# Optimization experiments

Hardware: AMD Instinct MI355X
Metric: run time of the kernel (lower is better)

## Reference

```python
import jax, jax.numpy as jnp
import numpy as np

WZ, WH, WW = 2, 6, 12  # window_size (Z, H, W)
NUM_HEADS = 6


def _layernorm(x, g, b, eps=1e-5):
    m = jnp.mean(x, axis=-1, keepdims=True)
    v = jnp.mean((x - m) ** 2, axis=-1, keepdims=True)
    return (x - m) * jax.lax.rsqrt(v + eps) * g + b


def setup_inputs() -> dict:
    key = jax.random.key(0)
    ks = jax.random.split(key, 8)
    B, Z, H, W, C = 1, 8, 91, 180, 192
    s = 0.02
    return {
        "x": jax.random.normal(ks[0], (B, Z * H * W, C), jnp.float32),
        "norm1_g": jnp.ones((C,), jnp.float32),
        "norm1_b": jnp.zeros((C,), jnp.float32),
        "qkv_w": jax.random.normal(ks[1], (3 * C, C), jnp.float32) * s,
        "qkv_b": jnp.zeros((3 * C,), jnp.float32),
        "proj_w": jax.random.normal(ks[2], (C, C), jnp.float32) * s,
        "proj_b": jnp.zeros((C,), jnp.float32),
        "norm2_g": jnp.ones((C,), jnp.float32),
        "norm2_b": jnp.zeros((C,), jnp.float32),
        "fc1_w": jax.random.normal(ks[3], (4 * C, C), jnp.float32) * s,
        "fc1_b": jnp.zeros((4 * C,), jnp.float32),
        "fc2_w": jax.random.normal(ks[4], (C, 4 * C), jnp.float32) * s,
        "fc2_b": jnp.zeros((C,), jnp.float32),
        "Z": Z, "H": H, "W": W, "roll": 1,
    }


def _forward(x, norm1_g, norm1_b, qkv_w, qkv_b, proj_w, proj_b,
             norm2_g, norm2_b, fc1_w, fc1_b, fc2_w, fc2_b, Z, H, W, roll):
    B, N, C = x.shape
    shortcut = x
    x = x.reshape(B, Z, H, W, C)
    # pad to window multiples (right-pad, as in torch F.pad)
    pz, ph, pw = (-Z) % WZ, (-H) % WH, (-W) % WW
    x = jnp.pad(x, ((0, 0), (0, pz), (0, ph), (0, pw), (0, 0)))
    Zp, Hp, Wp = Z + pz, H + ph, W + pw
    if roll:
        x = jnp.roll(x, (-(WZ // 2), -(WH // 2), -(WW // 2)), axis=(1, 2, 3))
    # window partition -> (B*nW, wz*wh*ww, C)
    x = x.reshape(B, Zp // WZ, WZ, Hp // WH, WH, Wp // WW, WW, C)
    x = x.transpose(0, 1, 3, 5, 2, 4, 6, 7).reshape(-1, WZ * WH * WW, C)
    xw = _layernorm(x, norm1_g, norm1_b)
    # windowed multi-head attention (mask is always None in this module)
    nw, L, _ = xw.shape
    hd = C // NUM_HEADS
    qkv = (xw @ qkv_w.T + qkv_b).reshape(nw, L, 3, NUM_HEADS, hd)
    q, k, v = jnp.moveaxis(qkv, 2, 0)        # each (nw, L, nh, hd)
    q = q * (hd ** -0.5)
    attn = jnp.einsum('nqhd,nkhd->nhqk', q, k)
    attn = jax.nn.softmax(attn, axis=-1)
    out = jnp.einsum('nhqk,nkhd->nqhd', attn, v).reshape(nw, L, C)
    out = out @ proj_w.T + proj_b
    # window reverse
    x = out.reshape(B, Zp // WZ, Hp // WH, Wp // WW, WZ, WH, WW, C)
    x = x.transpose(0, 1, 4, 2, 5, 3, 6, 7).reshape(B, Zp, Hp, Wp, C)
    if roll:
        x = jnp.roll(x, (WZ // 2, WH // 2, WW // 2), axis=(1, 2, 3))
    x = x[:, :Z, :H, :W, :].reshape(B, Z * H * W, C)
    x = shortcut + x
    # MLP with post-norm (as written in the source: x + norm2(mlp(x)))
    h = jax.nn.gelu(x @ fc1_w.T + fc1_b, approximate=False)
    h = h @ fc2_w.T + fc2_b
    return x + _layernorm(h, norm2_g, norm2_b)


def reference(x, norm1_g, norm1_b, qkv_w, qkv_b, proj_w, proj_b,
              norm2_g, norm2_b, fc1_w, fc1_b, fc2_w, fc2_b, Z, H, W, roll):
    return _forward(x, norm1_g, norm1_b, qkv_w, qkv_b, proj_w, proj_b,
                    norm2_g, norm2_b, fc1_w, fc1_b, fc2_w, fc2_b, Z, H, W, roll)
```

## Files before the change

kernel.cpp:

```cpp
#include <hip/hip_runtime.h>
#include <hip/hip_bf16.h>
#include <math.h>

#define C_DIM 192
#define NH 6
#define HD 32
#define L_WIN 144
#define NWIN 960
#define MROWS (NWIN * L_WIN)
#define NTOK 131040
#define Z_ 8
#define H_ 91
#define W_ 180
#define HP_ 96
#define WS_REQUIRED 212336640ull

#define OFF_WBF   0ull
#define OFF_XWC   1048576ull
#define OFF_QKVB  51367936ull
#define OFF_ATTNO 1048576ull
#define OFF_X1B   51367936ull
#define WO_QKV  0
#define WO_PROJ 110592
#define WO_FC1  147456
#define WO_FC2  294912
#define WO_BETA 442368
#define W_TOTAL 442560

typedef __attribute__((ext_vector_type(8))) short bf16x8;
typedef __attribute__((ext_vector_type(4))) float f32x4;

__device__ __forceinline__ short f2bf(float f) {
    union { __hip_bfloat16 h; short s; } u; u.h = __float2bfloat16(f); return u.s;
}
__device__ __forceinline__ float bf2f(short s) {
    return __uint_as_float(((unsigned int)(unsigned short)s) << 16);
}

__device__ __forceinline__ int win_token_to_tok(int r) {
    int n = r / L_WIN, l = r - n * L_WIN;
    int wz = n / 240;
    int rem = n - wz * 240;
    int wh = rem / 15;
    int ww = rem - wh * 15;
    int iz = l / 72;
    int r2 = l - iz * 72;
    int ih = r2 / 12;
    int iw = r2 - ih * 12;
    int z = wz * 2 + iz;
    int h = wh * 6 + ih;
    int w = ww * 12 + iw;
    int zp = z + 1; if (zp >= Z_) zp -= Z_;
    int hp = h + 3; if (hp >= HP_) hp -= HP_;
    int wp = w + 6; if (wp >= W_) wp -= W_;
    if (hp >= H_) return -1;
    return (zp * H_ + hp) * W_ + wp;
}

__global__ __launch_bounds__(256)
void wconv_kernel(const float* __restrict__ qw, const float* __restrict__ pw,
                  const float* __restrict__ f1w, const float* __restrict__ f2w,
                  const float* __restrict__ n1b, short* __restrict__ wbf) {
    int i = blockIdx.x * 256 + threadIdx.x;
    if (i >= W_TOTAL) return;
    float v;
    if (i < WO_PROJ)      v = qw[i];
    else if (i < WO_FC1)  v = pw[i - WO_PROJ];
    else if (i < WO_FC2)  v = f1w[i - WO_FC1];
    else if (i < WO_BETA) v = f2w[i - WO_FC2];
    else                  v = n1b[i - WO_BETA];
    wbf[i] = f2bf(v);
}

__global__ __launch_bounds__(256)
void ln_tok_kernel(const float* __restrict__ x, const float* __restrict__ g,
                   const float* __restrict__ b, short* __restrict__ xwc) {
    int wave = threadIdx.x >> 6, lane = threadIdx.x & 63;
    int r = blockIdx.x * 4 + wave;
    if (r >= NTOK) return;
    const float* p = x + (size_t)r * C_DIM;
    float v0 = p[lane], v1 = p[lane + 64], v2 = p[lane + 128];
    float s = v0 + v1 + v2;
    float sq = v0 * v0 + v1 * v1 + v2 * v2;
    #pragma unroll
    for (int off = 32; off; off >>= 1) {
        s += __shfl_xor(s, off);
        sq += __shfl_xor(sq, off);
    }
    float m = s * (1.f / 192.f);
    float var = sq * (1.f / 192.f) - m * m;
    float inv = rsqrtf(var + 1e-5f);
    short* o = xwc + (size_t)r * C_DIM;
    o[lane]       = f2bf((v0 - m) * inv * g[lane]       + b[lane]);
    o[lane + 64]  = f2bf((v1 - m) * inv * g[lane + 64]  + b[lane + 64]);
    o[lane + 128] = f2bf((v2 - m) * inv * g[lane + 128] + b[lane + 128]);
}

__global__ __launch_bounds__(256)
void qkv_gemm(const short* __restrict__ xwc, const short* __restrict__ wq,
              const short* __restrict__ beta, const float* __restrict__ bias,
              short* __restrict__ qkvb) {
    __shared__ __align__(16) short As[128][200];
    int t = threadIdx.x, w = t >> 6, l = t & 63, g = l >> 4, c = l & 15;
    int row0 = blockIdx.y * 128, col0 = blockIdx.x * 64;
    int wr = (w >> 1) * 64, wc = (w & 1) * 32;
    {
        int r = t & 127;
        int th = t >> 7;
        int tok = win_token_to_tok(row0 + r);
        const short* src = (tok >= 0) ? xwc + (size_t)tok * C_DIM : beta;
        #pragma unroll
        for (int i = 0; i < 12; i++) {
            int cidx = th + 2 * i;
            *(bf16x8*)(&As[r][cidx * 8]) = *(const bf16x8*)(src + cidx * 8);
        }
    }
    __syncthreads();
    f32x4 acc[4][2] = {};
    #pragma unroll
    for (int k0 = 0; k0 < 192; k0 += 32) {
        bf16x8 af[4], bfr[2];
        #pragma unroll
        for (int n = 0; n < 2; n++)
            bfr[n] = *(const bf16x8*)(wq + (size_t)(col0 + wc + 16 * n + c) * 192 + k0 + g * 8);
        #pragma unroll
        for (int m = 0; m < 4; m++) af[m] = *(const bf16x8*)(&As[wr + 16 * m + c][k0 + g * 8]);
        #pragma unroll
        for (int m = 0; m < 4; m++)
            #pragma unroll
            for (int n = 0; n < 2; n++)
                acc[m][n] = __builtin_amdgcn_mfma_f32_16x16x32_bf16(af[m], bfr[n], acc[m][n], 0, 0, 0);
    }
    #pragma unroll
    for (int m = 0; m < 4; m++)
        #pragma unroll
        for (int reg = 0; reg < 4; reg++) {
            int r = row0 + wr + 16 * m + 4 * g + reg;
            #pragma unroll
            for (int n = 0; n < 2; n++) {
                int col = col0 + wc + 16 * n + c;
                qkvb[(size_t)r * 576 + col] = f2bf(acc[m][n][reg] + bias[col]);
            }
        }
}

__global__ __launch_bounds__(256)
void attn_mfma(const short* __restrict__ qkv, short* __restrict__ attno) {
    __shared__ __align__(16) short Vt[32][168];
    __shared__ __align__(16) short Pl[4][16][168];
    int blk = blockIdx.x;
    int win = blk / NH, head = blk - win * NH;
    int t = threadIdx.x, w = t >> 6, l = t & 63, g = l >> 4, c = l & 15;
    const short* base = qkv + (size_t)win * L_WIN * 576 + head * HD;

    for (int ch = t; ch < 576; ch += 256) {
        int kv = ch >> 2, cc = (ch & 3) * 8;
        bf16x8 v = *(const bf16x8*)(base + kv * 576 + 384 + cc);
        #pragma unroll
        for (int j = 0; j < 8; j++) Vt[cc + j][kv] = v[j];
    }
    for (int i = t; i < 32 * 24; i += 256) Vt[i / 24][144 + i % 24] = 0;
    for (int i = l; i < 16 * 24; i += 64) Pl[w][i / 24][144 + i % 24] = 0;
    __syncthreads();

    bf16x8 kf[9];
    #pragma unroll
    for (int n = 0; n < 9; n++)
        kf[n] = *(const bf16x8*)(base + (16 * n + c) * 576 + 192 + g * 8);

    const float scale = 0.17677669529663687f;
    for (int m = w; m < 9; m += 4) {
        bf16x8 qf = *(const bf16x8*)(base + (16 * m + c) * 576 + g * 8);
        f32x4 s[9];
        #pragma unroll
        for (int n = 0; n < 9; n++) {
            f32x4 z = {};
            s[n] = __builtin_amdgcn_mfma_f32_16x16x32_bf16(qf, kf[n], z, 0, 0, 0);
        }
        float mx[4], rs[4];
        #pragma unroll
        for (int reg = 0; reg < 4; reg++) {
            float v = -1e30f;
            #pragma unroll
            for (int n = 0; n < 9; n++) { s[n][reg] *= scale; v = fmaxf(v, s[n][reg]); }
            #pragma unroll
            for (int off = 1; off <= 8; off <<= 1) v = fmaxf(v, __shfl_xor(v, off));
            mx[reg] = v;
        }
        #pragma unroll
        for (int reg = 0; reg < 4; reg++) {
            float acc = 0.f;
            #pragma unroll
            for (int n = 0; n < 9; n++) {
                float e = __expf(s[n][reg] - mx[reg]);
                s[n][reg] = e;
                acc += e;
            }
            #pragma unroll
            for (int off = 1; off <= 8; off <<= 1) acc += __shfl_xor(acc, off);
            rs[reg] = 1.f / acc;
        }
        #pragma unroll
        for (int n = 0; n < 9; n++)
            #pragma unroll
            for (int reg = 0; reg < 4; reg++)
                Pl[w][4 * g + reg][16 * n + c] = f2bf(s[n][reg]);
        asm volatile("s_waitcnt lgkmcnt(0)" ::: "memory");
        f32x4 o[2] = {};
        #pragma unroll
        for (int ks = 0; ks < 5; ks++) {
            bf16x8 pa = *(const bf16x8*)(&Pl[w][c][32 * ks + 8 * g]);
            #pragma unroll
            for (int df = 0; df < 2; df++) {
                bf16x8 vb = *(const bf16x8*)(&Vt[16 * df + c][32 * ks + 8 * g]);
                o[df] = __builtin_amdgcn_mfma_f32_16x16x32_bf16(pa, vb, o[df], 0, 0, 0);
            }
        }
        #pragma unroll
        for (int reg = 0; reg < 4; reg++) {
            int grow = win * L_WIN + 16 * m + 4 * g + reg;
            int tok = win_token_to_tok(grow);
            if (tok < 0) continue;
            #pragma unroll
            for (int df = 0; df < 2; df++)
                attno[(size_t)tok * C_DIM + head * HD + 16 * df + c] =
                    f2bf(o[df][reg] * rs[reg]);
        }
    }
}

__global__ __launch_bounds__(256)
void proj_gemm(const short* __restrict__ attno, const short* __restrict__ wp,
               const float* __restrict__ bias, const float* __restrict__ x,
               short* __restrict__ x1b) {
    __shared__ __align__(16) short As[128][200];
    int t = threadIdx.x, w = t >> 6, l = t & 63, g = l >> 4, c = l & 15;
    int row0 = blockIdx.y * 128, col0 = blockIdx.x * 64;
    int wr = (w >> 1) * 64, wc = (w & 1) * 32;
    {
        int r = t & 127;
        int th = t >> 7;
        int gr = row0 + r;
        #pragma unroll
        for (int i = 0; i < 12; i++) {
            int cidx = th + 2 * i;
            bf16x8 v = {};
            if (gr < NTOK) v = *(const bf16x8*)(attno + (size_t)gr * C_DIM + cidx * 8);
            *(bf16x8*)(&As[r][cidx * 8]) = v;
        }
    }
    __syncthreads();
    f32x4 acc[4][2] = {};
    #pragma unroll
    for (int k0 = 0; k0 < 192; k0 += 32) {
        bf16x8 af[4], bfr[2];
        #pragma unroll
        for (int n = 0; n < 2; n++)
            bfr[n] = *(const bf16x8*)(wp + (size_t)(col0 + wc + 16 * n + c) * 192 + k0 + g * 8);
        #pragma unroll
        for (int m = 0; m < 4; m++) af[m] = *(const bf16x8*)(&As[wr + 16 * m + c][k0 + g * 8]);
        #pragma unroll
        for (int m = 0; m < 4; m++)
            #pragma unroll
            for (int n = 0; n < 2; n++)
                acc[m][n] = __builtin_amdgcn_mfma_f32_16x16x32_bf16(af[m], bfr[n], acc[m][n], 0, 0, 0);
    }
    #pragma unroll
    for (int m = 0; m < 4; m++)
        #pragma unroll
        for (int reg = 0; reg < 4; reg++) {
            int r = row0 + wr + 16 * m + 4 * g + reg;
            if (r >= NTOK) continue;
            #pragma unroll
            for (int n = 0; n < 2; n++) {
                int col = col0 + wc + 16 * n + c;
                float v = acc[m][n][reg] + bias[col] + x[(size_t)r * C_DIM + col];
                x1b[(size_t)r * C_DIM + col] = f2bf(v);
            }
        }
}

__global__ __launch_bounds__(256)
void mlp_kernel(const short* __restrict__ x1b, const short* __restrict__ w1,
                const short* __restrict__ w2, const float* __restrict__ b1,
                const float* __restrict__ b2, const float* __restrict__ g2,
                const float* __restrict__ bb2, float* __restrict__ out) {
    __shared__ __align__(16) short As[64][200];
    __shared__ __align__(16) short Hs[64][200];
    __shared__ float red_s[64][4];
    __shared__ float red_q[64][4];
    int t = threadIdx.x, w = t >> 6, l = t & 63, g = l >> 4, c = l & 15;
    int row0 = blockIdx.x * 64;
    {
        int r = t & 63;
        int sg = t >> 6;
        int gr = row0 + r;
        #pragma unroll
        for (int i = 0; i < 6; i++) {
            int cidx = sg + 4 * i;
            bf16x8 v = {};
            if (gr < NTOK) v = *(const bf16x8*)(x1b + (size_t)gr * C_DIM + cidx * 8);
            *(bf16x8*)(&As[r][cidx * 8]) = v;
        }
    }
    __syncthreads();

    f32x4 acc2[4][3] = {};
    for (int q = 0; q < 4; q++) {
        f32x4 acc1[4][3] = {};
        #pragma unroll
        for (int k0 = 0; k0 < 192; k0 += 32) {
            bf16x8 af[4], bfr[3];
            #pragma unroll
            for (int n = 0; n < 3; n++)
                bfr[n] = *(const bf16x8*)(w1 + (size_t)(q * 192 + 48 * w + 16 * n + c) * 192 + k0 + g * 8);
            #pragma unroll
            for (int m = 0; m < 4; m++) af[m] = *(const bf16x8*)(&As[16 * m + c][k0 + g * 8]);
            #pragma unroll
            for (int m = 0; m < 4; m++)
                #pragma unroll
                for (int n = 0; n < 3; n++)
                    acc1[m][n] = __builtin_amdgcn_mfma_f32_16x16x32_bf16(af[m], bfr[n], acc1[m][n], 0, 0, 0);
        }
        #pragma unroll
        for (int m = 0; m < 4; m++)
            #pragma unroll
            for (int n = 0; n < 3; n++)
                #pragma unroll
                for (int reg = 0; reg < 4; reg++) {
                    int col = 48 * w + 16 * n + c;
                    float v = acc1[m][n][reg] + b1[q * 192 + col];
                    float u = v * (1.5957691216f + 0.0713548162f * v * v);
                    float e = exp2f(-1.4426950409f * u);
                    float gl = v * __builtin_amdgcn_rcpf(1.f + e);
                    Hs[16 * m + 4 * g + reg][col] = f2bf(gl);
                }
        __syncthreads();
        #pragma unroll
        for (int k0 = 0; k0 < 192; k0 += 32) {
            bf16x8 pa[4], bfr[3];
            #pragma unroll
            for (int n = 0; n < 3; n++)
                bfr[n] = *(const bf16x8*)(w2 + (size_t)(48 * w + 16 * n + c) * 768 + q * 192 + k0 + g * 8);
            #pragma unroll
            for (int m = 0; m < 4; m++) pa[m] = *(const bf16x8*)(&Hs[16 * m + c][k0 + g * 8]);
            #pragma unroll
            for (int m = 0; m < 4; m++)
                #pragma unroll
                for (int n = 0; n < 3; n++)
                    acc2[m][n] = __builtin_amdgcn_mfma_f32_16x16x32_bf16(pa[m], bfr[n], acc2[m][n], 0, 0, 0);
        }
        __syncthreads();
    }

    #pragma unroll
    for (int m = 0; m < 4; m++)
        #pragma unroll
        for (int reg = 0; reg < 4; reg++) {
            float s = 0.f, sq = 0.f;
            #pragma unroll
            for (int n = 0; n < 3; n++) {
                int col = 48 * w + 16 * n + c;
                float h = acc2[m][n][reg] + b2[col];
                acc2[m][n][reg] = h;
                s += h; sq += h * h;
            }
            #pragma unroll
            for (int off = 1; off <= 8; off <<= 1) {
                s += __shfl_xor(s, off);
                sq += __shfl_xor(sq, off);
            }
            if (c == 0) {
                int q16 = 16 * m + 4 * g + reg;
                red_s[q16][w] = s;
                red_q[q16][w] = sq;
            }
        }
    __syncthreads();
    #pragma unroll
    for (int m = 0; m < 4; m++)
        #pragma unroll
        for (int reg = 0; reg < 4; reg++) {
            int q16 = 16 * m + 4 * g + reg;
            int r = row0 + q16;
            float s = red_s[q16][0] + red_s[q16][1] + red_s[q16][2] + red_s[q16][3];
            float sq = red_q[q16][0] + red_q[q16][1] + red_q[q16][2] + red_q[q16][3];
            float mean = s * (1.f / 192.f);
            float var = sq * (1.f / 192.f) - mean * mean;
            float inv = rsqrtf(var + 1e-5f);
            if (r < NTOK) {
                #pragma unroll
                for (int n = 0; n < 3; n++) {
                    int col = 48 * w + 16 * n + c;
                    out[(size_t)r * C_DIM + col] =
                        bf2f(As[q16][col]) + (acc2[m][n][reg] - mean) * inv * g2[col] + bb2[col];
                }
            }
        }
}

extern "C" void kernel_launch(void* const* d_in, const int* in_sizes, int n_in,
                              void* d_out, int out_size, void* d_ws, size_t ws_size,
                              hipStream_t stream) {
    const float* x      = (const float*)d_in[0];
    const float* n1g    = (const float*)d_in[1];
    const float* n1b    = (const float*)d_in[2];
    const float* qkv_w  = (const float*)d_in[3];
    const float* qkv_b  = (const float*)d_in[4];
    const float* proj_w = (const float*)d_in[5];
    const float* proj_b = (const float*)d_in[6];
    const float* n2g    = (const float*)d_in[7];
    const float* n2b    = (const float*)d_in[8];
    const float* fc1_w  = (const float*)d_in[9];
    const float* fc1_b  = (const float*)d_in[10];
    const float* fc2_w  = (const float*)d_in[11];
    const float* fc2_b  = (const float*)d_in[12];
    float* out = (float*)d_out;

    if (ws_size < WS_REQUIRED) return;

    char* ws = (char*)d_ws;
    short* wbf   = (short*)(ws + OFF_WBF);
    short* xwc   = (short*)(ws + OFF_XWC);
    short* qkvb  = (short*)(ws + OFF_QKVB);
    short* attno = (short*)(ws + OFF_ATTNO);
    short* x1b   = (short*)(ws + OFF_X1B);

    wconv_kernel<<<(W_TOTAL + 255) / 256, 256, 0, stream>>>(
        qkv_w, proj_w, fc1_w, fc2_w, n1b, wbf);

    ln_tok_kernel<<<NTOK / 4, 256, 0, stream>>>(x, n1g, n1b, xwc);

    qkv_gemm<<<dim3(9, MROWS / 128), 256, 0, stream>>>(
        xwc, wbf + WO_QKV, wbf + WO_BETA, qkv_b, qkvb);

    attn_mfma<<<NWIN * NH, 256, 0, stream>>>(qkvb, attno);

    proj_gemm<<<dim3(3, (NTOK + 127) / 128), 256, 0, stream>>>(
        attno, wbf + WO_PROJ, proj_b, x, x1b);

    mlp_kernel<<<(NTOK + 63) / 64, 256, 0, stream>>>(
        x1b, wbf + WO_FC1, wbf + WO_FC2, fc1_b, fc2_b, n2g, n2b, out);
}
```

Before: 559.6 us.

## Remap GEMM blocks across XCDs, prefetch weights, head-major QKV layout, transposed fc1

The QKV GEMM now writes its output head-major (window, head, q/k/v, token, dim), so attention reads contiguous 32-wide rows. The attention kernel drops to 192 threads (3 waves over 9 row tiles) and folds log2(e) into the scale so it can use exp2f. The QKV and proj GEMMs remap block IDs so consecutive row tiles land on the same XCD for L2 locality. All GEMM loops register-double-buffer the weight fragments. The MLP computes fc1 transposed, so bias and GELU results are packed and stored to LDS as 4-wide vectors, at the cost of an extra barrier.

```diff
diff --git a/kernel.cpp b/kernel.cpp
--- a/kernel.cpp
+++ b/kernel.cpp
@@ -28,6 +28,7 @@
 #define W_TOTAL 442560
 
 typedef __attribute__((ext_vector_type(8))) short bf16x8;
+typedef __attribute__((ext_vector_type(4))) short s16x4;
 typedef __attribute__((ext_vector_type(4))) float f32x4;
 
 __device__ __forceinline__ short f2bf(float f) {
@@ -102,7 +103,10 @@
               short* __restrict__ qkvb) {
     __shared__ __align__(16) short As[128][200];
     int t = threadIdx.x, w = t >> 6, l = t & 63, g = l >> 4, c = l & 15;
-    int row0 = blockIdx.y * 128, col0 = blockIdx.x * 64;
+    int bid = blockIdx.x + 9 * blockIdx.y;
+    int xcd = bid & 7, sq_ = bid >> 3;
+    int bx = sq_ % 9, by = xcd + 8 * (sq_ / 9);
+    int row0 = by * 128, col0 = bx * 64;
     int wr = (w >> 1) * 64, wc = (w & 1) * 32;
     {
         int r = t & 127;
@@ -117,72 +121,89 @@
     }
     __syncthreads();
     f32x4 acc[4][2] = {};
-    #pragma unroll
-    for (int k0 = 0; k0 < 192; k0 += 32) {
-        bf16x8 af[4], bfr[2];
-        #pragma unroll
-        for (int n = 0; n < 2; n++)
-            bfr[n] = *(const bf16x8*)(wq + (size_t)(col0 + wc + 16 * n + c) * 192 + k0 + g * 8);
-        #pragma unroll
-        for (int m = 0; m < 4; m++) af[m] = *(const bf16x8*)(&As[wr + 16 * m + c][k0 + g * 8]);
+    const short* wqb = wq + (size_t)(col0 + wc + c) * 192 + g * 8;
+    bf16x8 cur[2], nxt[2];
+    #pragma unroll
+    for (int n = 0; n < 2; n++) cur[n] = *(const bf16x8*)(wqb + n * 3072);
+    #pragma unroll
+    for (int ks = 0; ks < 6; ks++) {
+        if (ks < 5) {
+            #pragma unroll
+            for (int n = 0; n < 2; n++)
+                nxt[n] = *(const bf16x8*)(wqb + n * 3072 + (ks + 1) * 32);
+        }
+        bf16x8 af[4];
         #pragma unroll
         for (int m = 0; m < 4; m++)
+            af[m] = *(const bf16x8*)(&As[wr + 16 * m + c][ks * 32 + g * 8]);
+        #pragma unroll
+        for (int m = 0; m < 4; m++)
             #pragma unroll
             for (int n = 0; n < 2; n++)
-                acc[m][n] = __builtin_amdgcn_mfma_f32_16x16x32_bf16(af[m], bfr[n], acc[m][n], 0, 0, 0);
+                acc[m][n] = __builtin_amdgcn_mfma_f32_16x16x32_bf16(af[m], cur[n], acc[m][n], 0, 0, 0);
+        if (ks < 5) {
+            #pragma unroll
+            for (int n = 0; n < 2; n++) cur[n] = nxt[n];
+        }
     }
     #pragma unroll
     for (int m = 0; m < 4; m++)
         #pragma unroll
         for (int reg = 0; reg < 4; reg++) {
             int r = row0 + wr + 16 * m + 4 * g + reg;
+            int win = r / 144, ll = r - win * 144;
             #pragma unroll
             for (int n = 0; n < 2; n++) {
                 int col = col0 + wc + 16 * n + c;
-                qkvb[(size_t)r * 576 + col] = f2bf(acc[m][n][reg] + bias[col]);
-            }
-        }
-}
-
-__global__ __launch_bounds__(256)
-void attn_mfma(const short* __restrict__ qkv, short* __restrict__ attno) {
+                int sec = col / 192;
+                int head = (col - sec * 192) >> 5;
+                int d = col & 31;
+                size_t dst = ((size_t)(win * 6 + head) * 3 + sec) * 4608 + ll * 32 + d;
+                qkvb[dst] = f2bf(acc[m][n][reg] + bias[col]);
+            }
+        }
+}
+
+__global__ __launch_bounds__(192)
+void attn_mfma(const short* __restrict__ qkvb, short* __restrict__ attno) {
     __shared__ __align__(16) short Vt[32][168];
-    __shared__ __align__(16) short Pl[4][16][168];
+    __shared__ __align__(16) short Pl[3][16][168];
     int blk = blockIdx.x;
     int win = blk / NH, head = blk - win * NH;
     int t = threadIdx.x, w = t >> 6, l = t & 63, g = l >> 4, c = l & 15;
-    const short* base = qkv + (size_t)win * L_WIN * 576 + head * HD;
-
-    for (int ch = t; ch < 576; ch += 256) {
+    const short* qb = qkvb + (size_t)(win * 6 + head) * 13824;
+    const short* kb = qb + 4608;
+    const short* vb = qb + 9216;
+    for (int ch = t; ch < 576; ch += 192) {
         int kv = ch >> 2, cc = (ch & 3) * 8;
-        bf16x8 v = *(const bf16x8*)(base + kv * 576 + 384 + cc);
+        bf16x8 v = *(const bf16x8*)(vb + kv * 32 + cc);
         #pragma unroll
         for (int j = 0; j < 8; j++) Vt[cc + j][kv] = v[j];
     }
-    for (int i = t; i < 32 * 24; i += 256) Vt[i / 24][144 + i % 24] = 0;
+    for (int i = t; i < 32 * 24; i += 192) Vt[i / 24][144 + i % 24] = 0;
     for (int i = l; i < 16 * 24; i += 64) Pl[w][i / 24][144 + i % 24] = 0;
     __syncthreads();
 
     bf16x8 kf[9];
     #pragma unroll
     for (int n = 0; n < 9; n++)
-        kf[n] = *(const bf16x8*)(base + (16 * n + c) * 576 + 192 + g * 8);
-
-    const float scale = 0.17677669529663687f;
-    for (int m = w; m < 9; m += 4) {
-        bf16x8 qf = *(const bf16x8*)(base + (16 * m + c) * 576 + g * 8);
-        f32x4 s[9];
+        kf[n] = *(const bf16x8*)(kb + (16 * n + c) * 32 + g * 8);
+
+    const float scale2 = 0.2550348668f;
+    for (int m = w; m < 9; m += 3) {
+        bf16x8 qf = *(const bf16x8*)(qb + (16 * m + c) * 32 + g * 8);
+        f32x4 sv[9];
         #pragma unroll
         for (int n = 0; n < 9; n++) {
             f32x4 z = {};
-            s[n] = __builtin_amdgcn_mfma_f32_16x16x32_bf16(qf, kf[n], z, 0, 0, 0);
+            sv[n] = __builtin_amdgcn_mfma_f32_16x16x32_bf16(qf, kf[n], z, 0, 0, 0);
         }
         float mx[4], rs[4];
         #pragma unroll
         for (int reg = 0; reg < 4; reg++) {
             float v = -1e30f;
             #pragma unroll
-            for (int n = 0; n < 9; n++) { s[n][reg] *= scale; v = fmaxf(v, s[n][reg]); }
+            for (int n = 0; n < 9; n++) { sv[n][reg] *= scale2; v = fmaxf(v, sv[n][reg]); }
             #pragma unroll
             for (int off = 1; off <= 8; off <<= 1) v = fmaxf(v, __shfl_xor(v, off));
             mx[reg] = v;
@@ -192,8 +213,8 @@
             float acc = 0.f;
             #pragma unroll
             for (int n = 0; n < 9; n++) {
-                float e = __expf(s[n][reg] - mx[reg]);
-                s[n][reg] = e;
+                float e = exp2f(sv[n][reg] - mx[reg]);
+                sv[n][reg] = e;
                 acc += e;
             }
             #pragma unroll
@@ -204,7 +225,7 @@
         for (int n = 0; n < 9; n++)
             #pragma unroll
             for (int reg = 0; reg < 4; reg++)
-                Pl[w][4 * g + reg][16 * n + c] = f2bf(s[n][reg]);
+                Pl[w][4 * g + reg][16 * n + c] = f2bf(sv[n][reg]);
         asm volatile("s_waitcnt lgkmcnt(0)" ::: "memory");
         f32x4 o[2] = {};
         #pragma unroll
@@ -212,8 +233,8 @@
             bf16x8 pa = *(const bf16x8*)(&Pl[w][c][32 * ks + 8 * g]);
             #pragma unroll
             for (int df = 0; df < 2; df++) {
-                bf16x8 vb = *(const bf16x8*)(&Vt[16 * df + c][32 * ks + 8 * g]);
-                o[df] = __builtin_amdgcn_mfma_f32_16x16x32_bf16(pa, vb, o[df], 0, 0, 0);
+                bf16x8 vv = *(const bf16x8*)(&Vt[16 * df + c][32 * ks + 8 * g]);
+                o[df] = __builtin_amdgcn_mfma_f32_16x16x32_bf16(pa, vv, o[df], 0, 0, 0);
             }
         }
         #pragma unroll
@@ -235,7 +256,10 @@
                short* __restrict__ x1b) {
     __shared__ __align__(16) short As[128][200];
     int t = threadIdx.x, w = t >> 6, l = t & 63, g = l >> 4, c = l & 15;
-    int row0 = blockIdx.y * 128, col0 = blockIdx.x * 64;
+    int bid = blockIdx.x + 3 * blockIdx.y;
+    int xcd = bid & 7, sq_ = bid >> 3;
+    int bx = sq_ % 3, by = xcd + 8 * (sq_ / 3);
+    int row0 = by * 128, col0 = bx * 64;
     int wr = (w >> 1) * 64, wc = (w & 1) * 32;
     {
         int r = t & 127;
@@ -251,19 +275,30 @@
     }
     __syncthreads();
     f32x4 acc[4][2] = {};
-    #pragma unroll
-    for (int k0 = 0; k0 < 192; k0 += 32) {
-        bf16x8 af[4], bfr[2];
-        #pragma unroll
-        for (int n = 0; n < 2; n++)
-            bfr[n] = *(const bf16x8*)(wp + (size_t)(col0 + wc + 16 * n + c) * 192 + k0 + g * 8);
-        #pragma unroll
-        for (int m = 0; m < 4; m++) af[m] = *(const bf16x8*)(&As[wr + 16 * m + c][k0 + g * 8]);
+    const short* wpb = wp + (size_t)(col0 + wc + c) * 192 + g * 8;
+    bf16x8 cur[2], nxt[2];
+    #pragma unroll
+    for (int n = 0; n < 2; n++) cur[n] = *(const bf16x8*)(wpb + n * 3072);
+    #pragma unroll
+    for (int ks = 0; ks < 6; ks++) {
+        if (ks < 5) {
+            #pragma unroll
+            for (int n = 0; n < 2; n++)
+                nxt[n] = *(const bf16x8*)(wpb + n * 3072 + (ks + 1) * 32);
+        }
+        bf16x8 af[4];
         #pragma unroll
         for (int m = 0; m < 4; m++)
+            af[m] = *(const bf16x8*)(&As[wr + 16 * m + c][ks * 32 + g * 8]);
+        #pragma unroll
+        for (int m = 0; m < 4; m++)
             #pragma unroll
             for (int n = 0; n < 2; n++)
-                acc[m][n] = __builtin_amdgcn_mfma_f32_16x16x32_bf16(af[m], bfr[n], acc[m][n], 0, 0, 0);
+                acc[m][n] = __builtin_amdgcn_mfma_f32_16x16x32_bf16(af[m], cur[n], acc[m][n], 0, 0, 0);
+        if (ks < 5) {
+            #pragma unroll
+            for (int n = 0; n < 2; n++) cur[n] = nxt[n];
+        }
     }
     #pragma unroll
     for (int m = 0; m < 4; m++)
@@ -292,8 +327,7 @@
     int t = threadIdx.x, w = t >> 6, l = t & 63, g = l >> 4, c = l & 15;
     int row0 = blockIdx.x * 64;
     {
-        int r = t & 63;
-        int sg = t >> 6;
+        int r = t & 63, sg = t >> 6;
         int gr = row0 + r;
         #pragma unroll
         for (int i = 0; i < 6; i++) {
@@ -307,50 +341,82 @@
 
     f32x4 acc2[4][3] = {};
     for (int q = 0; q < 4; q++) {
-        f32x4 acc1[4][3] = {};
-        #pragma unroll
-        for (int k0 = 0; k0 < 192; k0 += 32) {
-            bf16x8 af[4], bfr[3];
-            #pragma unroll
-            for (int n = 0; n < 3; n++)
-                bfr[n] = *(const bf16x8*)(w1 + (size_t)(q * 192 + 48 * w + 16 * n + c) * 192 + k0 + g * 8);
-            #pragma unroll
-            for (int m = 0; m < 4; m++) af[m] = *(const bf16x8*)(&As[16 * m + c][k0 + g * 8]);
-            #pragma unroll
-            for (int m = 0; m < 4; m++)
-                #pragma unroll
-                for (int n = 0; n < 3; n++)
-                    acc1[m][n] = __builtin_amdgcn_mfma_f32_16x16x32_bf16(af[m], bfr[n], acc1[m][n], 0, 0, 0);
-        }
-        #pragma unroll
-        for (int m = 0; m < 4; m++)
-            #pragma unroll
-            for (int n = 0; n < 3; n++)
+        const short* w1b = w1 + (size_t)(q * 192 + 48 * w + c) * 192 + g * 8;
+        f32x4 acc1[3][4] = {};
+        bf16x8 cur1[3], nxt1[3];
+        #pragma unroll
+        for (int mh = 0; mh < 3; mh++) cur1[mh] = *(const bf16x8*)(w1b + mh * 3072);
+        #pragma unroll
+        for (int ks = 0; ks < 6; ks++) {
+            if (ks < 5) {
+                #pragma unroll
+                for (int mh = 0; mh < 3; mh++)
+                    nxt1[mh] = *(const bf16x8*)(w1b + mh * 3072 + (ks + 1) * 32);
+            }
+            bf16x8 bx[4];
+            #pragma unroll
+            for (int tn = 0; tn < 4; tn++)
+                bx[tn] = *(const bf16x8*)(&As[16 * tn + c][ks * 32 + g * 8]);
+            #pragma unroll
+            for (int mh = 0; mh < 3; mh++)
+                #pragma unroll
+                for (int tn = 0; tn < 4; tn++)
+                    acc1[mh][tn] = __builtin_amdgcn_mfma_f32_16x16x32_bf16(cur1[mh], bx[tn], acc1[mh][tn], 0, 0, 0);
+            if (ks < 5) {
+                #pragma unroll
+                for (int mh = 0; mh < 3; mh++) cur1[mh] = nxt1[mh];
+            }
+        }
+        s16x4 pk[3][4];
+        #pragma unroll
+        for (int mh = 0; mh < 3; mh++) {
+            float bv[4];
+            #pragma unroll
+            for (int reg = 0; reg < 4; reg++)
+                bv[reg] = b1[q * 192 + 48 * w + 16 * mh + 4 * g + reg];
+            #pragma unroll
+            for (int tn = 0; tn < 4; tn++) {
                 #pragma unroll
                 for (int reg = 0; reg < 4; reg++) {
-                    int col = 48 * w + 16 * n + c;
-                    float v = acc1[m][n][reg] + b1[q * 192 + col];
+                    float v = acc1[mh][tn][reg] + bv[reg];
                     float u = v * (1.5957691216f + 0.0713548162f * v * v);
                     float e = exp2f(-1.4426950409f * u);
-                    float gl = v * __builtin_amdgcn_rcpf(1.f + e);
-                    Hs[16 * m + 4 * g + reg][col] = f2bf(gl);
+                    pk[mh][tn][reg] = f2bf(v * __builtin_amdgcn_rcpf(1.f + e));
                 }
+            }
+        }
         __syncthreads();
         #pragma unroll
-        for (int k0 = 0; k0 < 192; k0 += 32) {
-            bf16x8 pa[4], bfr[3];
-            #pragma unroll
-            for (int n = 0; n < 3; n++)
-                bfr[n] = *(const bf16x8*)(w2 + (size_t)(48 * w + 16 * n + c) * 768 + q * 192 + k0 + g * 8);
-            #pragma unroll
-            for (int m = 0; m < 4; m++) pa[m] = *(const bf16x8*)(&Hs[16 * m + c][k0 + g * 8]);
-            #pragma unroll
-            for (int m = 0; m < 4; m++)
+        for (int mh = 0; mh < 3; mh++)
+            #pragma unroll
+            for (int tn = 0; tn < 4; tn++)
+                *(s16x4*)(&Hs[16 * tn + c][48 * w + 16 * mh + 4 * g]) = pk[mh][tn];
+        __syncthreads();
+        const short* w2b = w2 + (size_t)(48 * w + c) * 768 + q * 192 + g * 8;
+        bf16x8 cur2[3], nxt2[3];
+        #pragma unroll
+        for (int n = 0; n < 3; n++) cur2[n] = *(const bf16x8*)(w2b + n * 12288);
+        #pragma unroll
+        for (int ks = 0; ks < 6; ks++) {
+            if (ks < 5) {
                 #pragma unroll
                 for (int n = 0; n < 3; n++)
-                    acc2[m][n] = __builtin_amdgcn_mfma_f32_16x16x32_bf16(pa[m], bfr[n], acc2[m][n], 0, 0, 0);
-        }
-        __syncthreads();
+                    nxt2[n] = *(const bf16x8*)(w2b + n * 12288 + (ks + 1) * 32);
+            }
+            bf16x8 pa[4];
+            #pragma unroll
+            for (int tm = 0; tm < 4; tm++)
+                pa[tm] = *(const bf16x8*)(&Hs[16 * tm + c][ks * 32 + g * 8]);
+            #pragma unroll
+            for (int tm = 0; tm < 4; tm++)
+                #pragma unroll
+                for (int n = 0; n < 3; n++)
+                    acc2[tm][n] = __builtin_amdgcn_mfma_f32_16x16x32_bf16(pa[tm], cur2[n], acc2[tm][n], 0, 0, 0);
+            if (ks < 5) {
+                #pragma unroll
+                for (int n = 0; n < 3; n++) cur2[n] = nxt2[n];
+            }
+        }
     }
 
     #pragma unroll
@@ -412,7 +478,7 @@
     const float* n2g    = (const float*)d_in[7];
     const float* n2b    = (const float*)d_in[8];
     const float* fc1_w  = (const float*)d_in[9];
-    const float* fc1_b  = (const float*)d_in[10];
+    const float* fc1_b_ = (const float*)d_in[10];
     const float* fc2_w  = (const float*)d_in[11];
     const float* fc2_b  = (const float*)d_in[12];
     float* out = (float*)d_out;
@@ -434,11 +500,11 @@
     qkv_gemm<<<dim3(9, MROWS / 128), 256, 0, stream>>>(
         xwc, wbf + WO_QKV, wbf + WO_BETA, qkv_b, qkvb);
 
-    attn_mfma<<<NWIN * NH, 256, 0, stream>>>(qkvb, attno);
+    attn_mfma<<<NWIN * NH, 192, 0, stream>>>(qkvb, attno);
 
     proj_gemm<<<dim3(3, (NTOK + 127) / 128), 256, 0, stream>>>(
         attno, wbf + WO_PROJ, proj_b, x, x1b);
 
     mlp_kernel<<<(NTOK + 63) / 64, 256, 0, stream>>>(
-        x1b, wbf + WO_FC1, wbf + WO_FC2, fc1_b, fc2_b, n2g, n2b, out);
-}
+        x1b, wbf + WO_FC1, wbf + WO_FC2, fc1_b_, fc2_b, n2g, n2b, out);
+}
```

Result: faster. 521.1 us (-6.9%).
